# Kernel tuning notes

Measured on AMD Instinct MI355X. Metric: run time of the kernel, lower is better.

## Reference

```python
import jax, jax.numpy as jnp
import numpy as np

E = 1024  # emb_dim

def _xavier(k, fan_in, fan_out):
    lim = float(np.sqrt(6.0 / (fan_in + fan_out)))
    return jax.random.uniform(k, (fan_out, fan_in), jnp.float32, -lim, lim)

def setup_inputs() -> dict:
    key = jax.random.key(0)
    ks = jax.random.split(key, 12)
    B, S, H = 2, 2048, 16
    inp = {
        "query": jax.random.normal(ks[0], (B, S, E), jnp.float32),
        "key": jax.random.normal(ks[1], (B, S, E), jnp.float32),
        "value": jax.random.normal(ks[2], (B, S, E), jnp.float32),
        "mask": jax.random.bernoulli(ks[3], 0.5, (B, S, S)),
        "num_heads": H,
        "Wq": _xavier(ks[4], E, E), "bq": jnp.zeros((E,), jnp.float32),
        "Wk": _xavier(ks[5], E, E), "bk": jnp.zeros((E,), jnp.float32),
        "Wv": _xavier(ks[6], E, E), "bv": jnp.zeros((E,), jnp.float32),
        "Wo": _xavier(ks[7], E, E), "bo": jnp.zeros((E,), jnp.float32),
    }
    return inp

def reference(query, key, value, mask, num_heads, Wq, bq, Wk, bk, Wv, bv, Wo, bo):
    B, S, Emb = query.shape
    H = num_heads
    d = Emb // H
    scale = jnp.sqrt(jnp.asarray(d, query.dtype))

    def split_heads(x, W, b):
        x = x @ W.T + b                       # [B,S,E]
        x = x.reshape(B, S, H, d)             # view(B,-1,H,d)
        return jnp.transpose(x, (0, 2, 1, 3)) # [B,H,S,d]

    q = split_heads(query, Wq, bq)
    k = split_heads(key, Wk, bk)
    v = split_heads(value, Wv, bv)

    scores = jnp.einsum('bhqd,bhkd->bhqk', q, k) / scale  # [B,H,S,S]
    scores = jnp.where(mask[:, None, :, :], jnp.asarray(-1e18, scores.dtype), scores)
    attn = jax.nn.softmax(scores, axis=-1)                # [B,H,S,S]
    out = jnp.einsum('bhqk,bhkd->bhqd', attn, v)          # [B,H,S,d]

    # faithful replication of the original's (buggy) reshapes:
    # bmm output layout is [B*H, S, d]; viewed as (H, B, S, d), permuted (0,2,1,3),
    # then flattened to (B, S, H*d).
    out = out.reshape(B * H, S, d)
    out = out.reshape(H, B, S, d)
    out = jnp.transpose(out, (0, 2, 1, 3)).reshape(B, S, H * d)
    out = out @ Wo.T + bo
    return out, attn.reshape(B * H, S, S)
```

## Files before the change

kernel.cpp:

```cpp
#include <hip/hip_runtime.h>
#include <stdint.h>

typedef __attribute__((ext_vector_type(4))) float f32x4;
typedef __attribute__((ext_vector_type(8))) short short8;
typedef unsigned short u16;
typedef unsigned int u32;
typedef unsigned long long u64;

#define GLDS16(g, l) __builtin_amdgcn_global_load_lds( \
    (const __attribute__((address_space(1))) void*)(g), \
    (__attribute__((address_space(3))) void*)(l), 16, 0, 0)

#define ORDER_FENCE() asm volatile("" ::: "memory")

#if __has_builtin(__builtin_amdgcn_exp2f)
#define EXP2(x) __builtin_amdgcn_exp2f(x)
#else
#define EXP2(x) __expf(0.69314718056f * (x))
#endif

__device__ __forceinline__ u16 f2bf(float x) {
  u32 u = __float_as_uint(x);
  u += 0x7fffu + ((u >> 16) & 1u);
  return (u16)(u >> 16);
}

__global__ __launch_bounds__(256) void prep_kernel(
    const float* __restrict__ q, const float* __restrict__ k,
    const float* __restrict__ v, const int* __restrict__ mask,
    const float* __restrict__ Wq, const float* __restrict__ Wk,
    const float* __restrict__ Wv, const float* __restrict__ Wo,
    u16* __restrict__ X, u16* __restrict__ Wb, u64* __restrict__ mb)
{
  const size_t tid = (size_t)blockIdx.x * 256 + threadIdx.x;
  const size_t nth = (size_t)gridDim.x * 256;
  for (size_t i = tid; i < 3ull * 524288ull; i += nth) {
    const int a = (int)(i / 524288ull);
    const size_t j = i - (size_t)a * 524288ull;
    const float4* s4 = (const float4*)(a == 0 ? q : a == 1 ? k : v);
    float4 x = s4[2 * j], y = s4[2 * j + 1];
    uint4 o;
    o.x = (u32)f2bf(x.x) | ((u32)f2bf(x.y) << 16);
    o.y = (u32)f2bf(x.z) | ((u32)f2bf(x.w) << 16);
    o.z = (u32)f2bf(y.x) | ((u32)f2bf(y.y) << 16);
    o.w = (u32)f2bf(y.z) | ((u32)f2bf(y.w) << 16);
    ((uint4*)X)[i] = o;
  }
  for (size_t i = tid; i < 4ull * 131072ull; i += nth) {
    const int a = (int)(i / 131072ull);
    const size_t j = i - (size_t)a * 131072ull;
    const float4* s4 = (const float4*)(a == 0 ? Wq : a == 1 ? Wk : a == 2 ? Wv : Wo);
    float4 x = s4[2 * j], y = s4[2 * j + 1];
    uint4 o;
    o.x = (u32)f2bf(x.x) | ((u32)f2bf(x.y) << 16);
    o.y = (u32)f2bf(x.z) | ((u32)f2bf(x.w) << 16);
    o.z = (u32)f2bf(y.x) | ((u32)f2bf(y.y) << 16);
    o.w = (u32)f2bf(y.z) | ((u32)f2bf(y.w) << 16);
    ((uint4*)Wb)[i] = o;
  }
  const int lane = threadIdx.x & 63;
  const size_t wid = tid >> 6, nw = nth >> 6;
  for (size_t wi = wid; wi < 131072ull; wi += nw) {
    int mm = mask[wi * 64 + lane];
    u64 bal = __ballot(mm != 0);
    if (lane == 0) mb[wi] = bal;
  }
}

__global__ __launch_bounds__(256, 2) void gemm_qkv_kernel(
    const u16* __restrict__ X, const u16* __restrict__ W,
    const float* __restrict__ bq, const float* __restrict__ bk,
    const float* __restrict__ bv,
    u16* __restrict__ Qb, u16* __restrict__ Kb, u16* __restrict__ Vt)
{
  const int lid = blockIdx.x;
  const int g = (lid & 7) * 96 + (lid >> 3);
  const int z = g >> 8;
  const int rem = g & 255;
  const int m0 = (rem >> 3) * 128, n0 = (rem & 7) * 128;
  const char* A = (const char*)(X + (size_t)z * 4194304ull);
  const char* B = (const char*)(W + (size_t)z * 1048576ull);
  const float* bias = (z == 0) ? bq : (z == 1) ? bk : bv;
  const int tid = threadIdx.x, l = tid & 63, w = tid >> 6;
  const int wm = w >> 1, wn = w & 1;
  __shared__ __attribute__((aligned(16))) char SM[32768];
  char* Asm = SM;
  char* Bsm = SM + 16384;
  f32x4 acc[4][4] = {};
  for (int kt = 0; kt < 16; ++kt) {
#pragma unroll
    for (int j = 0; j < 4; ++j) {
      const int rt = w * 32 + j * 8 + (l >> 3);
      const int swk = ((l & 7) * 16) ^ ((rt & 7) << 4);
      GLDS16(A + (size_t)(m0 + rt) * 2048 + kt * 128 + swk, Asm + (w * 32 + j * 8) * 128);
      GLDS16(B + (size_t)(n0 + rt) * 2048 + kt * 128 + swk, Bsm + (w * 32 + j * 8) * 128);
    }
    __syncthreads();
#pragma unroll
    for (int kk = 0; kk < 2; ++kk) {
      short8 af[4], bfr[4];
#pragma unroll
      for (int mf = 0; mf < 4; ++mf) {
        const int row = wm * 64 + mf * 16 + (l & 15);
        const int kb = kk * 64 + (l >> 4) * 16;
        af[mf] = *(const short8*)(Asm + row * 128 + (kb ^ ((row & 7) << 4)));
      }
#pragma unroll
      for (int fc = 0; fc < 4; ++fc) {
        const int row = wn * 64 + fc * 16 + (l & 15);
        const int kb = kk * 64 + (l >> 4) * 16;
        bfr[fc] = *(const short8*)(Bsm + row * 128 + (kb ^ ((row & 7) << 4)));
      }
#pragma unroll
      for (int mf = 0; mf < 4; ++mf)
#pragma unroll
        for (int fc = 0; fc < 4; ++fc)
          acc[mf][fc] = __builtin_amdgcn_mfma_f32_16x16x32_bf16(af[mf], bfr[fc], acc[mf][fc], 0, 0, 0);
    }
    __syncthreads();
  }
  if (z < 2) {
    const float scale = (z == 0) ? 0.18033688011f : 1.0f;
    u16* dst = (z == 0) ? Qb : Kb;
#pragma unroll
    for (int mf = 0; mf < 4; ++mf)
#pragma unroll
      for (int fc = 0; fc < 4; ++fc)
#pragma unroll
        for (int r = 0; r < 4; ++r) {
          const int m = m0 + wm * 64 + mf * 16 + (l >> 4) * 4 + r;
          const int n = n0 + wn * 64 + fc * 16 + (l & 15);
          const float val = (acc[mf][fc][r] + bias[n]) * scale;
          const int bb = m >> 11, s = m & 2047;
          const int hh = n >> 6, dd = n & 63;
          dst[((size_t)(bb * 16 + hh) * 2048 + s) * 64 + dd] = f2bf(val);
        }
  } else {
#pragma unroll
    for (int mf = 0; mf < 4; ++mf)
#pragma unroll
      for (int fc = 0; fc < 4; ++fc)
#pragma unroll
        for (int r = 0; r < 4; ++r) {
          const int n_l = wn * 64 + fc * 16 + (l & 15);
          const int m_l = wm * 64 + mf * 16 + (l >> 4) * 4 + r;
          const float val = acc[mf][fc][r] + bias[n0 + n_l];
          *(u16*)(SM + n_l * 256 + ((m_l * 2) ^ ((n_l & 15) << 4))) = f2bf(val);
        }
    __syncthreads();
    const int bb = m0 >> 11, ms = m0 & 2047;
#pragma unroll
    for (int rep = 0; rep < 8; ++rep) {
      const int n_l = rep * 16 + (tid >> 4);
      const int m8 = (tid & 15) * 8;
      const uint4 dv = *(const uint4*)(SM + n_l * 256 + ((m8 * 2) ^ ((n_l & 15) << 4)));
      const int hh = (n0 + n_l) >> 6, dd = (n0 + n_l) & 63;
      *(uint4*)(Vt + ((size_t)((bb * 16 + hh) * 64 + dd)) * 2048 + ms + m8) = dv;
    }
  }
}

__global__ __launch_bounds__(256, 4) void lsum_kernel(
    const u16* __restrict__ Qb, const u16* __restrict__ Kb,
    const u32* __restrict__ mbits, float* __restrict__ lrow)
{
  const int lid = blockIdx.x;
  const int g = (lid & 7) * 128 + (lid >> 3);
  const int bh = g >> 5, qb = g & 31;
  const int b = bh >> 4;
  const int q0 = qb * 64;
  const int tid = threadIdx.x, l = tid & 63, w = tid >> 6;

  __shared__ __attribute__((aligned(16))) char kbuf[2][16384];
  __shared__ float rbuf[4][64];

  const char* Qrow = (const char*)(Qb + (size_t)bh * 131072ull);
  const char* Krow = (const char*)(Kb + (size_t)bh * 131072ull);

  short8 aq[4][2];
#pragma unroll
  for (int qf = 0; qf < 4; ++qf)
#pragma unroll
    for (int kk = 0; kk < 2; ++kk)
      aq[qf][kk] = *(const short8*)(Qrow + (size_t)(q0 + qf * 16 + (l & 15)) * 128 +
                                    kk * 64 + (l >> 4) * 16);
  const u32* mbase[4];
#pragma unroll
  for (int qf = 0; qf < 4; ++qf)
    mbase[qf] = mbits + (size_t)(b * 2048 + q0 + qf * 16 + (l & 15)) * 64 + w;

  ORDER_FENCE();
#pragma unroll
  for (int j = 0; j < 4; ++j) {
    const int row = j * 32 + w * 8 + (l >> 3);
    GLDS16(Krow + (size_t)row * 128 + (((l & 7) * 16) ^ ((row & 7) << 4)),
           kbuf[0] + j * 4096 + w * 1024);
  }
  ORDER_FENCE();
  u32 mreg[4];
#pragma unroll
  for (int qf = 0; qf < 4; ++qf) mreg[qf] = mbase[qf][0];

  float lsum[4] = {0.f, 0.f, 0.f, 0.f};
  for (int t = 0; t < 16; ++t) {
    asm volatile("s_waitcnt vmcnt(4) lgkmcnt(0)" ::: "memory");
    __builtin_amdgcn_s_barrier();
    u32 mnext[4] = {0, 0, 0, 0};
    if (t < 15) {
      ORDER_FENCE();
#pragma unroll
      for (int j = 0; j < 4; ++j) {
        const int row = j * 32 + w * 8 + (l >> 3);
        GLDS16(Krow + (size_t)((t + 1) * 128 + row) * 128 + (((l & 7) * 16) ^ ((row & 7) << 4)),
               kbuf[(t + 1) & 1] + j * 4096 + w * 1024);
      }
      ORDER_FENCE();
#pragma unroll
      for (int qf = 0; qf < 4; ++qf) mnext[qf] = mbase[qf][(t + 1) * 4];
    }
#pragma unroll
    for (int i = 0; i < 2; ++i) {
      const int krow = (w * 2 + i) * 16 + (l & 15);
      short8 ak[2];
#pragma unroll
      for (int kk = 0; kk < 2; ++kk)
        ak[kk] = *(const short8*)(kbuf[t & 1] + krow * 128 +
                                  ((kk * 64 + (l >> 4) * 16) ^ ((krow & 7) << 4)));
#pragma unroll
      for (int qf = 0; qf < 4; ++qf) {
        f32x4 sc = {0.f, 0.f, 0.f, 0.f};
        sc = __builtin_amdgcn_mfma_f32_16x16x32_bf16(ak[0], aq[qf][0], sc, 0, 0, 0);
        sc = __builtin_amdgcn_mfma_f32_16x16x32_bf16(ak[1], aq[qf][1], sc, 0, 0, 0);
        const int bp = i * 16 + (l >> 4) * 4;
        float s = 0.f;
#pragma unroll
        for (int r = 0; r < 4; ++r)
          s += ((mreg[qf] >> (bp + r)) & 1u) ? 0.f : EXP2(sc[r]);
        lsum[qf] += s;
      }
    }
#pragma unroll
    for (int qf = 0; qf < 4; ++qf) mreg[qf] = mnext[qf];
  }
#pragma unroll
  for (int qf = 0; qf < 4; ++qf) {
    float v = lsum[qf];
    v += __shfl_xor(v, 16);
    v += __shfl_xor(v, 32);
    if (l < 16) rbuf[w][qf * 16 + l] = v;
  }
  __syncthreads();
  if (tid < 64)
    lrow[(size_t)bh * 2048 + q0 + tid] =
        rbuf[0][tid] + rbuf[1][tid] + rbuf[2][tid] + rbuf[3][tid];
}

__global__ __launch_bounds__(512, 4) void attn_kernel(
    const u16* __restrict__ Qb, const u16* __restrict__ Kb,
    const u16* __restrict__ Vt, const u32* __restrict__ mbits,
    const float* __restrict__ lrow, float* __restrict__ attn,
    u16* __restrict__ preWo)
{
  const int lid = blockIdx.x;
  const int swz = (lid & 7) * 64 + (lid >> 3);
  const int bh = swz >> 4, qb = swz & 15;
  const int b = bh >> 4, h = bh & 15;
  const int q0 = qb * 128;
  const int tid = threadIdx.x, l = tid & 63, w = tid >> 6;
  const int wk = w & 3, wqh = w >> 2;
  const int wq = w >> 1, wd = w & 1;

  __shared__ __attribute__((aligned(16))) char kbuf[2][8192];
  __shared__ __attribute__((aligned(16))) char vbuf[3][8192];
  __shared__ __attribute__((aligned(16))) char Psm[2][16384];

  const char* Qrow = (const char*)(Qb + (size_t)bh * 131072ull);
  const char* Krow = (const char*)(Kb + (size_t)bh * 131072ull);
  const char* Vrow = (const char*)(Vt + (size_t)bh * 131072ull);

  {
    const int row = tid >> 3, byte = (tid & 7) * 16;
    GLDS16(Qrow + (size_t)(q0 + row) * 128 + (byte ^ ((row & 7) << 4)), Psm[0] + w * 1024);
    const int row2 = 64 + row;
    GLDS16(Qrow + (size_t)(q0 + row2) * 128 + (byte ^ ((row2 & 7) << 4)), Psm[0] + 8192 + w * 1024);
    GLDS16(Krow + (size_t)row * 128 + (byte ^ ((row & 7) << 4)), kbuf[0] + w * 1024);
    GLDS16(Vrow + (size_t)row * 4096 + (byte ^ ((row & 7) << 4)), vbuf[0] + w * 1024);
  }
  __syncthreads();
  short8 aq[4][2];
#pragma unroll
  for (int qf = 0; qf < 4; ++qf)
#pragma unroll
    for (int kk = 0; kk < 2; ++kk) {
      const int row = wqh * 64 + qf * 16 + (l & 15);
      aq[qf][kk] = *(const short8*)(Psm[0] + row * 128 +
                                    ((kk * 64 + (l >> 4) * 16) ^ ((row & 7) << 4)));
    }
  float il[4];
#pragma unroll
  for (int qf = 0; qf < 4; ++qf) {
    const float lv = lrow[(size_t)bh * 2048 + q0 + wqh * 64 + qf * 16 + (l & 15)];
    il[qf] = (lv > 0.f) ? 1.0f / lv : 0.f;
  }
  __syncthreads();

  const u32* mbase[4];
#pragma unroll
  for (int qf = 0; qf < 4; ++qf)
    mbase[qf] = mbits + (size_t)(b * 2048 + q0 + wqh * 64 + qf * 16 + (l & 15)) * 64 + (wk >> 1);
  u32 mreg[4];
#pragma unroll
  for (int qf = 0; qf < 4; ++qf) mreg[qf] = mbase[qf][0];

  f32x4 oacc[2][2] = {};
  const int kbit = (wk & 1) * 16 + (l >> 4) * 4;
  int vstage = 1, vprev = 2;
  for (int t = 0; t < 32; ++t) {
    if (t == 1) {
      asm volatile("s_waitcnt vmcnt(4) lgkmcnt(0)" ::: "memory");
      __builtin_amdgcn_s_barrier();
    } else if (t >= 2) {
      asm volatile("s_waitcnt vmcnt(8) lgkmcnt(0)" ::: "memory");
      __builtin_amdgcn_s_barrier();
    }
    u32 mnext[4] = {0, 0, 0, 0};
    if (t < 31) {
      const int row = tid >> 3, byte = (tid & 7) * 16;
      ORDER_FENCE();
      GLDS16(Krow + (size_t)((t + 1) * 64 + row) * 128 + (byte ^ ((row & 7) << 4)),
             kbuf[(t + 1) & 1] + w * 1024);
      GLDS16(Vrow + (size_t)row * 4096 + (t + 1) * 128 + (byte ^ ((row & 7) << 4)),
             vbuf[vstage] + w * 1024);
      ORDER_FENCE();
#pragma unroll
      for (int qf = 0; qf < 4; ++qf) mnext[qf] = mbase[qf][(t + 1) * 2];
      ORDER_FENCE();
    }
    if (t > 0) {
      const char* Pp = Psm[(t - 1) & 1];
#pragma unroll
      for (int it = 0; it < 4; ++it) {
        const int q = w * 16 + it * 4 + (l >> 4);
        const uint2 pv = *(const uint2*)(Pp + q * 128 + (((l & 15) * 8) ^ ((q & 7) << 4)));
        f32x4 o;
        o[0] = __uint_as_float(pv.x << 16);
        o[1] = __uint_as_float(pv.x & 0xffff0000u);
        o[2] = __uint_as_float(pv.y << 16);
        o[3] = __uint_as_float(pv.y & 0xffff0000u);
        __builtin_nontemporal_store(o, (f32x4*)(attn +
            ((size_t)bh * 2048 + q0 + q) * 2048 + (t - 1) * 64 + (l & 15) * 4));
      }
    }
    short8 ak[2];
    {
      const int krow = wk * 16 + (l & 15);
      ak[0] = *(const short8*)(kbuf[t & 1] + krow * 128 +
                               (((l >> 4) * 16) ^ ((krow & 7) << 4)));
      ak[1] = *(const short8*)(kbuf[t & 1] + krow * 128 +
                               ((64 + (l >> 4) * 16) ^ ((krow & 7) << 4)));
    }
#pragma unroll
    for (int qf = 0; qf < 4; ++qf) {
      f32x4 sc = {0.f, 0.f, 0.f, 0.f};
      sc = __builtin_amdgcn_mfma_f32_16x16x32_bf16(ak[0], aq[qf][0], sc, 0, 0, 0);
      sc = __builtin_amdgcn_mfma_f32_16x16x32_bf16(ak[1], aq[qf][1], sc, 0, 0, 0);
      const int q = wqh * 64 + qf * 16 + (l & 15);
      float p[4];
#pragma unroll
      for (int r = 0; r < 4; ++r)
        p[r] = ((mreg[qf] >> (kbit + r)) & 1u) ? 0.f : EXP2(sc[r]) * il[qf];
      uint2 pk;
      pk.x = (u32)f2bf(p[0]) | ((u32)f2bf(p[1]) << 16);
      pk.y = (u32)f2bf(p[2]) | ((u32)f2bf(p[3]) << 16);
      *(uint2*)(Psm[t & 1] + q * 128 + ((wk * 32 + (l >> 4) * 8) ^ ((q & 7) << 4))) = pk;
    }
#pragma unroll
    for (int qf = 0; qf < 4; ++qf) mreg[qf] = mnext[qf];
    if (t > 0) {
      const char* Pp = Psm[(t - 1) & 1];
#pragma unroll
      for (int ka = 0; ka < 2; ++ka) {
        short8 pa[2], vb[2];
#pragma unroll
        for (int i = 0; i < 2; ++i) {
          const int qr = wq * 32 + i * 16 + (l & 15);
          pa[i] = *(const short8*)(Pp + qr * 128 +
                                   ((ka * 64 + (l >> 4) * 16) ^ ((qr & 7) << 4)));
        }
#pragma unroll
        for (int j = 0; j < 2; ++j) {
          const int dr = wd * 32 + j * 16 + (l & 15);
          vb[j] = *(const short8*)(vbuf[vprev] + dr * 128 +
                                   ((ka * 64 + (l >> 4) * 16) ^ ((dr & 7) << 4)));
        }
#pragma unroll
        for (int i = 0; i < 2; ++i)
#pragma unroll
          for (int j = 0; j < 2; ++j)
            oacc[i][j] = __builtin_amdgcn_mfma_f32_16x16x32_bf16(pa[i], vb[j], oacc[i][j], 0, 0, 0);
      }
    }
    vstage = (vstage == 2) ? 0 : vstage + 1;
    vprev = (vprev == 2) ? 0 : vprev + 1;
  }

  asm volatile("s_waitcnt lgkmcnt(0)" ::: "memory");
  __builtin_amdgcn_s_barrier();
  {
    const char* Pp = Psm[1];
#pragma unroll
    for (int it = 0; it < 4; ++it) {
      const int q = w * 16 + it * 4 + (l >> 4);
      const uint2 pv = *(const uint2*)(Pp + q * 128 + (((l & 15) * 8) ^ ((q & 7) << 4)));
      f32x4 o;
      o[0] = __uint_as_float(pv.x << 16);
      o[1] = __uint_as_float(pv.x & 0xffff0000u);
      o[2] = __uint_as_float(pv.y << 16);
      o[3] = __uint_as_float(pv.y & 0xffff0000u);
      __builtin_nontemporal_store(o, (f32x4*)(attn +
          ((size_t)bh * 2048 + q0 + q) * 2048 + 31 * 64 + (l & 15) * 4));
    }
#pragma unroll
    for (int ka = 0; ka < 2; ++ka) {
      short8 pa[2], vb[2];
#pragma unroll
      for (int i = 0; i < 2; ++i) {
        const int qr = wq * 32 + i * 16 + (l & 15);
        pa[i] = *(const short8*)(Pp + qr * 128 +
                                 ((ka * 64 + (l >> 4) * 16) ^ ((qr & 7) << 4)));
      }
#pragma unroll
      for (int j = 0; j < 2; ++j) {
        const int dr = wd * 32 + j * 16 + (l & 15);
        vb[j] = *(const short8*)(vbuf[1] + dr * 128 +
                                 ((ka * 64 + (l >> 4) * 16) ^ ((dr & 7) << 4)));
      }
#pragma unroll
      for (int i = 0; i < 2; ++i)
#pragma unroll
        for (int j = 0; j < 2; ++j)
          oacc[i][j] = __builtin_amdgcn_mfma_f32_16x16x32_bf16(pa[i], vb[j], oacc[i][j], 0, 0, 0);
    }
  }

#pragma unroll
  for (int i = 0; i < 2; ++i)
#pragma unroll
    for (int j = 0; j < 2; ++j)
#pragma unroll
      for (int r = 0; r < 4; ++r) {
        const int qg = q0 + wq * 32 + i * 16 + (l >> 4) * 4 + r;
        const int dd = wd * 32 + j * 16 + (l & 15);
        const size_t off = (size_t)b * 2097152ull +
                           ((size_t)((h >> 1) * 256 + (qg >> 3))) * 1024ull +
                           (size_t)((qg & 7) * 128 + (h & 1) * 64 + dd);
        preWo[off] = f2bf(oacc[i][j][r]);
      }
}

__global__ __launch_bounds__(256, 2) void gemm_out_kernel(
    const u16* __restrict__ A0, const u16* __restrict__ B0,
    const float* __restrict__ bias, float* __restrict__ out)
{
  const char* A = (const char*)A0;
  const char* B = (const char*)B0;
  const int lid = blockIdx.x;
  const int g = (lid & 7) * 64 + (lid >> 3);
  const int m0 = (g >> 4) * 128, n0 = (g & 15) * 64;
  const int tid = threadIdx.x, l = tid & 63, w = tid >> 6;
  const int wm = w >> 1, wn = w & 1;
  __shared__ __attribute__((aligned(16))) char SM[24576];
  char* Asm = SM;
  char* Bsm = SM + 16384;
  f32x4 acc[4][2] = {};
  for (int kt = 0; kt < 16; ++kt) {
#pragma unroll
    for (int j = 0; j < 4; ++j) {
      const int rt = w * 32 + j * 8 + (l >> 3);
      const int swk = ((l & 7) * 16) ^ ((rt & 7) << 4);
      GLDS16(A + (size_t)(m0 + rt) * 2048 + kt * 128 + swk, Asm + (w * 32 + j * 8) * 128);
    }
#pragma unroll
    for (int j = 0; j < 2; ++j) {
      const int rt = w * 16 + j * 8 + (l >> 3);
      const int swk = ((l & 7) * 16) ^ ((rt & 7) << 4);
      GLDS16(B + (size_t)(n0 + rt) * 2048 + kt * 128 + swk, Bsm + (w * 16 + j * 8) * 128);
    }
    __syncthreads();
#pragma unroll
    for (int kk = 0; kk < 2; ++kk) {
      short8 af[4], bfr[2];
#pragma unroll
      for (int mf = 0; mf < 4; ++mf) {
        const int row = wm * 64 + mf * 16 + (l & 15);
        const int kb = kk * 64 + (l >> 4) * 16;
        af[mf] = *(const short8*)(Asm + row * 128 + (kb ^ ((row & 7) << 4)));
      }
#pragma unroll
      for (int fc = 0; fc < 2; ++fc) {
        const int row = wn * 32 + fc * 16 + (l & 15);
        const int kb = kk * 64 + (l >> 4) * 16;
        bfr[fc] = *(const short8*)(Bsm + row * 128 + (kb ^ ((row & 7) << 4)));
      }
#pragma unroll
      for (int mf = 0; mf < 4; ++mf)
#pragma unroll
        for (int fc = 0; fc < 2; ++fc)
          acc[mf][fc] = __builtin_amdgcn_mfma_f32_16x16x32_bf16(af[mf], bfr[fc], acc[mf][fc], 0, 0, 0);
    }
    __syncthreads();
  }
#pragma unroll
  for (int mf = 0; mf < 4; ++mf)
#pragma unroll
    for (int fc = 0; fc < 2; ++fc)
#pragma unroll
      for (int r = 0; r < 4; ++r) {
        const int m = m0 + wm * 64 + mf * 16 + (l >> 4) * 4 + r;
        const int n = n0 + wn * 32 + fc * 16 + (l & 15);
        out[(size_t)m * 1024 + n] = acc[mf][fc][r] + bias[n];
      }
}

extern "C" void kernel_launch(void* const* d_in, const int* in_sizes, int n_in,
                              void* d_out, int out_size, void* d_ws, size_t ws_size,
                              hipStream_t stream) {
  const float* q  = (const float*)d_in[0];
  const float* k  = (const float*)d_in[1];
  const float* v  = (const float*)d_in[2];
  const int*  mask = (const int*)d_in[3];
  const float* Wq = (const float*)d_in[5];
  const float* bq = (const float*)d_in[6];
  const float* Wk = (const float*)d_in[7];
  const float* bk = (const float*)d_in[8];
  const float* Wv = (const float*)d_in[9];
  const float* bv = (const float*)d_in[10];
  const float* Wo = (const float*)d_in[11];
  const float* bo = (const float*)d_in[12];

  float* out0 = (float*)d_out;
  float* attn = out0 + 4194304;
  u16* X = (u16*)attn;
  char* ws = (char*)d_ws;
  u16* Qb    = (u16*)(ws);
  u16* Kb    = (u16*)(ws + 8388608);
  u16* Vt    = (u16*)(ws + 16777216);
  u16* preWo = (u16*)(ws + 25165824);
  u16* Wb    = (u16*)(ws + 33554432);
  u32* mbits = (u32*)(ws + 41943040);
  float* lrow = (float*)(ws + 33554432);

  prep_kernel<<<dim3(1024), 256, 0, stream>>>(q, k, v, mask, Wq, Wk, Wv, Wo,
                                              X, Wb, (u64*)mbits);
  gemm_qkv_kernel<<<dim3(768), 256, 0, stream>>>(X, Wb, bq, bk, bv, Qb, Kb, Vt);
  lsum_kernel<<<dim3(1024), 256, 0, stream>>>(Qb, Kb, mbits, lrow);
  attn_kernel<<<dim3(512), 512, 0, stream>>>(Qb, Kb, Vt, mbits, lrow, attn, preWo);
  gemm_out_kernel<<<dim3(512), 256, 0, stream>>>(preWo, Wb + 3u * 1048576u, bo, out0);
}
```

Measured before the change: 244.5 us.

## Restructure lsum kernel to 128-query tiles with 512 threads and LDS-staged Q

The row-sum (softmax denominator) kernel now handles 128 query rows per block with 8 waves instead of 64 rows with 4 waves. Each K tile of 64 keys is loaded once into LDS and shared by twice as many queries, which halves global K traffic. Q is staged through swizzled LDS rather than read directly from global memory, and the grid is halved to match attn_kernel's tiling. The cost is more loop iterations with smaller per-step K tiles, and one extra barrier for the Q staging.

```diff
diff --git a/kernel.cpp b/kernel.cpp
--- a/kernel.cpp
+++ b/kernel.cpp
@@ -160,84 +160,86 @@
   }
 }
 
-__global__ __launch_bounds__(256, 4) void lsum_kernel(
+__global__ __launch_bounds__(512, 4) void lsum_kernel(
     const u16* __restrict__ Qb, const u16* __restrict__ Kb,
     const u32* __restrict__ mbits, float* __restrict__ lrow)
 {
   const int lid = blockIdx.x;
-  const int g = (lid & 7) * 128 + (lid >> 3);
-  const int bh = g >> 5, qb = g & 31;
+  const int swz = (lid & 7) * 64 + (lid >> 3);
+  const int bh = swz >> 4, qb = swz & 15;
   const int b = bh >> 4;
-  const int q0 = qb * 64;
+  const int q0 = qb * 128;
   const int tid = threadIdx.x, l = tid & 63, w = tid >> 6;
-
-  __shared__ __attribute__((aligned(16))) char kbuf[2][16384];
-  __shared__ float rbuf[4][64];
+  const int wk = w & 3, wqh = w >> 2;
+
+  __shared__ __attribute__((aligned(16))) char kbuf[2][8192];
+  __shared__ __attribute__((aligned(16))) char Qsm[16384];
+  __shared__ float rbuf[8][64];
 
   const char* Qrow = (const char*)(Qb + (size_t)bh * 131072ull);
   const char* Krow = (const char*)(Kb + (size_t)bh * 131072ull);
 
+  {
+    const int row = tid >> 3, byte = (tid & 7) * 16;
+    GLDS16(Qrow + (size_t)(q0 + row) * 128 + (byte ^ ((row & 7) << 4)), Qsm + w * 1024);
+    const int row2 = 64 + row;
+    GLDS16(Qrow + (size_t)(q0 + row2) * 128 + (byte ^ ((row2 & 7) << 4)), Qsm + 8192 + w * 1024);
+    GLDS16(Krow + (size_t)row * 128 + (byte ^ ((row & 7) << 4)), kbuf[0] + w * 1024);
+  }
+  __syncthreads();
   short8 aq[4][2];
 #pragma unroll
   for (int qf = 0; qf < 4; ++qf)
 #pragma unroll
-    for (int kk = 0; kk < 2; ++kk)
-      aq[qf][kk] = *(const short8*)(Qrow + (size_t)(q0 + qf * 16 + (l & 15)) * 128 +
-                                    kk * 64 + (l >> 4) * 16);
+    for (int kk = 0; kk < 2; ++kk) {
+      const int row = wqh * 64 + qf * 16 + (l & 15);
+      aq[qf][kk] = *(const short8*)(Qsm + row * 128 +
+                                    ((kk * 64 + (l >> 4) * 16) ^ ((row & 7) << 4)));
+    }
+
   const u32* mbase[4];
 #pragma unroll
   for (int qf = 0; qf < 4; ++qf)
-    mbase[qf] = mbits + (size_t)(b * 2048 + q0 + qf * 16 + (l & 15)) * 64 + w;
-
-  ORDER_FENCE();
-#pragma unroll
-  for (int j = 0; j < 4; ++j) {
-    const int row = j * 32 + w * 8 + (l >> 3);
-    GLDS16(Krow + (size_t)row * 128 + (((l & 7) * 16) ^ ((row & 7) << 4)),
-           kbuf[0] + j * 4096 + w * 1024);
-  }
+    mbase[qf] = mbits + (size_t)(b * 2048 + q0 + wqh * 64 + qf * 16 + (l & 15)) * 64 + (wk >> 1);
   ORDER_FENCE();
   u32 mreg[4];
 #pragma unroll
   for (int qf = 0; qf < 4; ++qf) mreg[qf] = mbase[qf][0];
 
   float lsum[4] = {0.f, 0.f, 0.f, 0.f};
-  for (int t = 0; t < 16; ++t) {
+  const int kbit = (wk & 1) * 16 + (l >> 4) * 4;
+  for (int t = 0; t < 32; ++t) {
     asm volatile("s_waitcnt vmcnt(4) lgkmcnt(0)" ::: "memory");
     __builtin_amdgcn_s_barrier();
     u32 mnext[4] = {0, 0, 0, 0};
-    if (t < 15) {
+    if (t < 31) {
+      const int row = tid >> 3, byte = (tid & 7) * 16;
       ORDER_FENCE();
-#pragma unroll
-      for (int j = 0; j < 4; ++j) {
-        const int row = j * 32 + w * 8 + (l >> 3);
-        GLDS16(Krow + (size_t)((t + 1) * 128 + row) * 128 + (((l & 7) * 16) ^ ((row & 7) << 4)),
-               kbuf[(t + 1) & 1] + j * 4096 + w * 1024);
-      }
+      GLDS16(Krow + (size_t)((t + 1) * 64 + row) * 128 + (byte ^ ((row & 7) << 4)),
+             kbuf[(t + 1) & 1] + w * 1024);
       ORDER_FENCE();
 #pragma unroll
-      for (int qf = 0; qf < 4; ++qf) mnext[qf] = mbase[qf][(t + 1) * 4];
-    }
-#pragma unroll
-    for (int i = 0; i < 2; ++i) {
-      const int krow = (w * 2 + i) * 16 + (l & 15);
-      short8 ak[2];
-#pragma unroll
-      for (int kk = 0; kk < 2; ++kk)
-        ak[kk] = *(const short8*)(kbuf[t & 1] + krow * 128 +
-                                  ((kk * 64 + (l >> 4) * 16) ^ ((krow & 7) << 4)));
-#pragma unroll
-      for (int qf = 0; qf < 4; ++qf) {
-        f32x4 sc = {0.f, 0.f, 0.f, 0.f};
-        sc = __builtin_amdgcn_mfma_f32_16x16x32_bf16(ak[0], aq[qf][0], sc, 0, 0, 0);
-        sc = __builtin_amdgcn_mfma_f32_16x16x32_bf16(ak[1], aq[qf][1], sc, 0, 0, 0);
-        const int bp = i * 16 + (l >> 4) * 4;
-        float s = 0.f;
-#pragma unroll
-        for (int r = 0; r < 4; ++r)
-          s += ((mreg[qf] >> (bp + r)) & 1u) ? 0.f : EXP2(sc[r]);
-        lsum[qf] += s;
-      }
+      for (int qf = 0; qf < 4; ++qf) mnext[qf] = mbase[qf][(t + 1) * 2];
+      ORDER_FENCE();
+    }
+    short8 ak[2];
+    {
+      const int krow = wk * 16 + (l & 15);
+      ak[0] = *(const short8*)(kbuf[t & 1] + krow * 128 +
+                               (((l >> 4) * 16) ^ ((krow & 7) << 4)));
+      ak[1] = *(const short8*)(kbuf[t & 1] + krow * 128 +
+                               ((64 + (l >> 4) * 16) ^ ((krow & 7) << 4)));
+    }
+#pragma unroll
+    for (int qf = 0; qf < 4; ++qf) {
+      f32x4 sc = {0.f, 0.f, 0.f, 0.f};
+      sc = __builtin_amdgcn_mfma_f32_16x16x32_bf16(ak[0], aq[qf][0], sc, 0, 0, 0);
+      sc = __builtin_amdgcn_mfma_f32_16x16x32_bf16(ak[1], aq[qf][1], sc, 0, 0, 0);
+      float s = 0.f;
+#pragma unroll
+      for (int r = 0; r < 4; ++r)
+        s += ((mreg[qf] >> (kbit + r)) & 1u) ? 0.f : EXP2(sc[r]);
+      lsum[qf] += s;
     }
 #pragma unroll
     for (int qf = 0; qf < 4; ++qf) mreg[qf] = mnext[qf];
@@ -250,9 +252,12 @@
     if (l < 16) rbuf[w][qf * 16 + l] = v;
   }
   __syncthreads();
-  if (tid < 64)
+  if (tid < 128) {
+    const int half = tid >> 6, qi = tid & 63;
     lrow[(size_t)bh * 2048 + q0 + tid] =
-        rbuf[0][tid] + rbuf[1][tid] + rbuf[2][tid] + rbuf[3][tid];
+        rbuf[half * 4 + 0][qi] + rbuf[half * 4 + 1][qi] +
+        rbuf[half * 4 + 2][qi] + rbuf[half * 4 + 3][qi];
+  }
 }
 
 __global__ __launch_bounds__(512, 4) void attn_kernel(
@@ -553,7 +558,7 @@
   prep_kernel<<<dim3(1024), 256, 0, stream>>>(q, k, v, mask, Wq, Wk, Wv, Wo,
                                               X, Wb, (u64*)mbits);
   gemm_qkv_kernel<<<dim3(768), 256, 0, stream>>>(X, Wb, bq, bk, bv, Qb, Kb, Vt);
-  lsum_kernel<<<dim3(1024), 256, 0, stream>>>(Qb, Kb, mbits, lrow);
+  lsum_kernel<<<dim3(512), 512, 0, stream>>>(Qb, Kb, mbits, lrow);
   attn_kernel<<<dim3(512), 512, 0, stream>>>(Qb, Kb, Vt, mbits, lrow, attn, preWo);
   gemm_out_kernel<<<dim3(512), 256, 0, stream>>>(preWo, Wb + 3u * 1048576u, bo, out0);
 }
```

After: 261.3 us. +6.9%, slower.
